# Kernel optimization log

Hardware: AMD Instinct MI355X
Metric: run time of the kernel (lower is better)

## Reference

```python
import jax, jax.numpy as jnp
import numpy as np
import math

EMBED_DIM = 2048
NUM_HEADS = 32
NUM_KV_HEADS = 8
HEAD_DIM = EMBED_DIM // NUM_HEADS  # 64
N_REP = NUM_HEADS // NUM_KV_HEADS  # 4
BATCH = 2
SEQ = 2048


def _rope_tables(seq_len, head_dim):
    # standard RoPE tables matching rotate_half convention (frequencies tiled twice)
    inv_freq = 1.0 / (10000.0 ** (np.arange(0, head_dim, 2, dtype=np.float32) / head_dim))
    t = np.arange(seq_len, dtype=np.float32)
    freqs = np.outer(t, inv_freq)                      # (seq, head_dim/2)
    emb = np.concatenate([freqs, freqs], axis=-1)      # (seq, head_dim)
    return jnp.asarray(np.cos(emb)), jnp.asarray(np.sin(emb))


def setup_inputs() -> dict:
    key = jax.random.key(0)
    ks = jax.random.split(key, 6)
    scale = 1.0 / math.sqrt(EMBED_DIM)
    x = jax.random.normal(ks[0], (BATCH, SEQ, EMBED_DIM), dtype=jnp.float32)
    wq = jax.random.normal(ks[1], (EMBED_DIM, EMBED_DIM), dtype=jnp.float32) * scale
    wk = jax.random.normal(ks[2], (NUM_KV_HEADS * HEAD_DIM, EMBED_DIM), dtype=jnp.float32) * scale
    wv = jax.random.normal(ks[3], (NUM_KV_HEADS * HEAD_DIM, EMBED_DIM), dtype=jnp.float32) * scale
    wo = jax.random.normal(ks[4], (EMBED_DIM, EMBED_DIM), dtype=jnp.float32) * scale
    freqs_cos, freqs_sin = _rope_tables(SEQ, HEAD_DIM)
    return {"x": x, "freqs_cos": freqs_cos, "freqs_sin": freqs_sin,
            "wq": wq, "wk": wk, "wv": wv, "wo": wo}


def _rotate_half(t):
    h = t.shape[-1] // 2
    return jnp.concatenate([-t[..., h:], t[..., :h]], axis=-1)


def reference(x, freqs_cos, freqs_sin, wq, wk, wv, wo):
    b, s, _ = x.shape
    # QKV projections (Linear with weight (out,in): y = x @ W^T)
    xq = (x @ wq.T).reshape(b, s, NUM_HEADS, HEAD_DIM).transpose(0, 2, 1, 3)     # (b,H,s,d)
    xk = (x @ wk.T).reshape(b, s, NUM_KV_HEADS, HEAD_DIM).transpose(0, 2, 1, 3)  # (b,Hkv,s,d)
    xv = (x @ wv.T).reshape(b, s, NUM_KV_HEADS, HEAD_DIM).transpose(0, 2, 1, 3)
    # RoPE: cos/sin (s,d) broadcast over (b,h,s,d)
    xq = xq * freqs_cos + _rotate_half(xq) * freqs_sin
    xk = xk * freqs_cos + _rotate_half(xk) * freqs_sin
    # GQA: repeat_interleave kv heads to match q heads
    xk = jnp.repeat(xk, N_REP, axis=1)  # (b,H,s,d)
    xv = jnp.repeat(xv, N_REP, axis=1)
    scores = jnp.einsum('bhqd,bhkd->bhqk', xq, xk) / math.sqrt(HEAD_DIM)
    causal = jnp.tril(jnp.ones((s, s), dtype=bool))
    scores = jnp.where(causal, scores, jnp.float32(-1e30))
    attn = jax.nn.softmax(scores, axis=-1)
    out = jnp.einsum('bhqk,bhkd->bhqd', attn, xv)        # (b,H,s,d)
    out = out.transpose(0, 2, 1, 3).reshape(b, s, EMBED_DIM)
    return out @ wo.T
```

## Files before the change

kernel.cpp:

```cpp
#include <hip/hip_runtime.h>

#define BATCH 2
#define SEQ 2048
#define EMBED 2048
#define NHEADS 32
#define NKV 8
#define HDIM 64
#define QKV_LD 3072
#define LOG2E 1.44269504088896f

typedef __attribute__((ext_vector_type(8))) short short8;
typedef __attribute__((ext_vector_type(4))) float f32x4;

__device__ inline float hw_exp2(float x) { return __builtin_amdgcn_exp2f(x); }

__device__ inline ushort f2bf(float f) {
  union { float f; unsigned u; } v{f};
  unsigned r = v.u + 0x7FFF + ((v.u >> 16) & 1);
  return (ushort)(r >> 16);
}
__device__ inline float bf2f(ushort u) {
  union { unsigned u; float f; } v{((unsigned)u) << 16};
  return v.f;
}
__device__ inline unsigned fbits(float f) {
  union { float f; unsigned u; } v{f};
  return v.u;
}

__device__ inline void gload16(const ushort* g, ushort* l) {
  __builtin_amdgcn_global_load_lds(
      (const __attribute__((address_space(1))) unsigned*)g,
      (__attribute__((address_space(3))) unsigned*)l, 16, 0, 0);
}

__global__ __launch_bounds__(256) void cvt_all(const float* __restrict__ x,
                                               const float* __restrict__ wq,
                                               const float* __restrict__ wk,
                                               const float* __restrict__ wv,
                                               const float* __restrict__ wo,
                                               ushort* __restrict__ xb,
                                               ushort* __restrict__ wqkv,
                                               ushort* __restrict__ wob) {
  size_t e = (size_t)(blockIdx.x * blockDim.x + threadIdx.x) * 8;
  const float* src;
  ushort* dst;
  if (e < 8388608u) { src = x + e; dst = xb + e; }
  else if (e < 12582912u) { size_t o = e - 8388608u; src = wq + o; dst = wqkv + o; }
  else if (e < 13631488u) { size_t o = e - 12582912u; src = wk + o; dst = wqkv + 4194304u + o; }
  else if (e < 14680064u) { size_t o = e - 13631488u; src = wv + o; dst = wqkv + 5242880u + o; }
  else { size_t o = e - 14680064u; src = wo + o; dst = wob + o; }
  float4 v0 = ((const float4*)src)[0];
  float4 v1 = ((const float4*)src)[1];
  union { uint4 v; ushort u[8]; } pk;
  pk.u[0] = f2bf(v0.x); pk.u[1] = f2bf(v0.y); pk.u[2] = f2bf(v0.z); pk.u[3] = f2bf(v0.w);
  pk.u[4] = f2bf(v1.x); pk.u[5] = f2bf(v1.y); pk.u[6] = f2bf(v1.z); pk.u[7] = f2bf(v1.w);
  *(uint4*)dst = pk.v;
}

template <typename OutT>
__global__ __launch_bounds__(256) void gemm_bf16(const ushort* __restrict__ A,
                                                 const ushort* __restrict__ B,
                                                 OutT* __restrict__ C,
                                                 int M, int N, int K) {
  __shared__ ushort As[128][32];
  __shared__ ushort Bs[128][32];
  const int tid = threadIdx.x;
  const int lane = tid & 63, wave = tid >> 6;
  const int quad = lane >> 4, l16 = lane & 15;
  const int m0 = blockIdx.y * 128, n0 = blockIdx.x * 128;
  const int wm = (wave >> 1) * 64, wn = (wave & 1) * 64;
  const int srow = lane >> 2, skq = (lane & 3) * 8;

  f32x4 acc[4][4] = {};
  for (int k0 = 0; k0 < K; k0 += 32) {
    const ushort* ga = A + (size_t)(m0 + wave * 32 + srow) * K + k0 + skq;
    const ushort* gb = B + (size_t)(n0 + wave * 32 + srow) * K + k0 + skq;
    __syncthreads();
    gload16(ga, &As[wave * 32][0]);
    gload16(ga + (size_t)16 * K, &As[wave * 32 + 16][0]);
    gload16(gb, &Bs[wave * 32][0]);
    gload16(gb + (size_t)16 * K, &Bs[wave * 32 + 16][0]);
    __syncthreads();
    short8 af[4], bf[4];
#pragma unroll
    for (int i = 0; i < 4; i++) af[i] = *(short8*)&As[wm + i * 16 + l16][quad * 8];
#pragma unroll
    for (int j = 0; j < 4; j++) bf[j] = *(short8*)&Bs[wn + j * 16 + l16][quad * 8];
#pragma unroll
    for (int i = 0; i < 4; i++)
#pragma unroll
      for (int j = 0; j < 4; j++)
        acc[i][j] = __builtin_amdgcn_mfma_f32_16x16x32_bf16(af[i], bf[j], acc[i][j], 0, 0, 0);
  }
#pragma unroll
  for (int i = 0; i < 4; i++) {
#pragma unroll
    for (int r = 0; r < 4; r++) {
      size_t rg = (size_t)(m0 + wm + i * 16 + quad * 4 + r);
#pragma unroll
      for (int j = 0; j < 4; j++) {
        float v = acc[i][j][r];
        int cg = n0 + wn + j * 16 + l16;
        if constexpr (sizeof(OutT) == 2)
          C[rg * N + cg] = f2bf(v);
        else
          C[rg * N + cg] = v;
      }
    }
  }
}

__global__ __launch_bounds__(256) void rope_qk(ushort* __restrict__ t,
                                               const float* __restrict__ fc,
                                               const float* __restrict__ fs,
                                               int total) {
  int idx = blockIdx.x * blockDim.x + threadIdx.x;
  if (idx >= total) return;
  int g = idx & 3;
  int hh = (idx >> 2) % 40;
  int tok = idx / 160;
  int s = tok & (SEQ - 1);
  float scale = (hh < 32) ? 0.125f * LOG2E : 1.0f;
  ushort* p = t + (size_t)tok * QKV_LD + hh * 64 + g * 8;
  union { uint4 v; ushort u[8]; } lo, hi, olo, ohi;
  lo.v = *(const uint4*)p;
  hi.v = *(const uint4*)(p + 32);
  const float* fcb = fc + s * HDIM + g * 8;
  const float* fsb = fs + s * HDIM + g * 8;
  float4 c0a = ((const float4*)fcb)[0], c0b = ((const float4*)fcb)[1];
  float4 s0a = ((const float4*)fsb)[0], s0b = ((const float4*)fsb)[1];
  float4 c1a = ((const float4*)(fcb + 32))[0], c1b = ((const float4*)(fcb + 32))[1];
  float4 s1a = ((const float4*)(fsb + 32))[0], s1b = ((const float4*)(fsb + 32))[1];
  float cc0[8] = {c0a.x, c0a.y, c0a.z, c0a.w, c0b.x, c0b.y, c0b.z, c0b.w};
  float ss0[8] = {s0a.x, s0a.y, s0a.z, s0a.w, s0b.x, s0b.y, s0b.z, s0b.w};
  float cc1[8] = {c1a.x, c1a.y, c1a.z, c1a.w, c1b.x, c1b.y, c1b.z, c1b.w};
  float ss1[8] = {s1a.x, s1a.y, s1a.z, s1a.w, s1b.x, s1b.y, s1b.z, s1b.w};
#pragma unroll
  for (int j = 0; j < 8; j++) {
    float x0 = bf2f(lo.u[j]), x1 = bf2f(hi.u[j]);
    olo.u[j] = f2bf((x0 * cc0[j] - x1 * ss0[j]) * scale);
    ohi.u[j] = f2bf((x1 * cc1[j] + x0 * ss1[j]) * scale);
  }
  *(uint4*)p = olo.v;
  *(uint4*)(p + 32) = ohi.v;
}

__global__ __launch_bounds__(256) void attn_mfma(const ushort* __restrict__ QKV,
                                                 ushort* __restrict__ O) {
  __shared__ ushort Ks[64][72];
  __shared__ ushort Vt[64][72];
  __shared__ ushort Pw[4][16][72];
  const int tid = threadIdx.x;
  const int lane = tid & 63, wave = tid >> 6;
  const int quad = lane >> 4, l16 = lane & 15;
  const int bh = blockIdx.y;
  const int b = bh >> 5, h = bh & 31, kh = h >> 2;
  const int p = blockIdx.x;
  const int qt[2] = {p, 31 - p};
  const int ntiles = 32 - p;

  short8 qf[2][2];
#pragma unroll
  for (int u = 0; u < 2; u++)
#pragma unroll
    for (int c = 0; c < 2; c++)
      qf[u][c] = *(const short8*)(QKV +
          (size_t)(b * SEQ + qt[u] * 64 + wave * 16 + l16) * QKV_LD +
          h * HDIM + c * 32 + quad * 8);

  f32x4 o[2][4] = {};
  float m[2] = {-INFINITY, -INFINITY}, l[2] = {0.f, 0.f};

  const ushort* Kbase = QKV + (size_t)b * SEQ * QKV_LD + 2048 + kh * HDIM;
  const ushort* Vbase = Kbase + 512;
  const int kp = tid & 31, dg = tid >> 5;
  const int relrow = wave * 16 + l16;

  for (int t = 0; t < ntiles; t++) {
    const int k0 = t * 64;
    __syncthreads();
    {
      const float4* kpp = (const float4*)(Kbase + (size_t)(k0 + lane) * QKV_LD + wave * 16);
      float4 kv0 = kpp[0], kv1 = kpp[1];
      const uint4* va4 = (const uint4*)(Vbase + (size_t)(k0 + 2 * kp) * QKV_LD + dg * 8);
      const uint4* vb4 = (const uint4*)(Vbase + (size_t)(k0 + 2 * kp + 1) * QKV_LD + dg * 8);
      uint4 va = va4[0], vb = vb4[0];
      *(float4*)&Ks[lane][wave * 16] = kv0;
      *(float4*)&Ks[lane][wave * 16 + 8] = kv1;
      const unsigned* vaw = (const unsigned*)&va;
      const unsigned* vbw = (const unsigned*)&vb;
#pragma unroll
      for (int j = 0; j < 8; j++) {
        unsigned pk = (j & 1)
            ? __builtin_amdgcn_perm(vbw[j >> 1], vaw[j >> 1], 0x07060302)
            : __builtin_amdgcn_perm(vbw[j >> 1], vaw[j >> 1], 0x05040100);
        *(unsigned*)&Vt[dg * 8 + j][2 * kp] = pk;
      }
    }
    __syncthreads();

#pragma unroll
    for (int u = 0; u < 2; u++) {
      const int diag = qt[u];
      if (t > diag) continue;

      f32x4 s[4];
#pragma unroll
      for (int nt = 0; nt < 4; nt++) {
        short8 kf0 = *(short8*)&Ks[nt * 16 + l16][quad * 8];
        short8 kf1 = *(short8*)&Ks[nt * 16 + l16][32 + quad * 8];
        f32x4 z = {};
        z = __builtin_amdgcn_mfma_f32_16x16x32_bf16(kf0, qf[u][0], z, 0, 0, 0);
        s[nt] = __builtin_amdgcn_mfma_f32_16x16x32_bf16(kf1, qf[u][1], z, 0, 0, 0);
      }

      if (t == diag) {
#pragma unroll
        for (int nt = 0; nt < 4; nt++)
#pragma unroll
          for (int r = 0; r < 4; r++)
            if (nt * 16 + quad * 4 + r > relrow) s[nt][r] = -INFINITY;
      }

      float mx = -INFINITY;
#pragma unroll
      for (int nt = 0; nt < 4; nt++)
#pragma unroll
        for (int r = 0; r < 4; r++) mx = fmaxf(mx, s[nt][r]);
      mx = fmaxf(mx, __shfl_xor(mx, 16));
      mx = fmaxf(mx, __shfl_xor(mx, 32));
      float mnew = fmaxf(m[u], mx);
      float al = hw_exp2(m[u] - mnew);
      m[u] = mnew;

      float pv[16];
      float psum = 0.f;
#pragma unroll
      for (int nt = 0; nt < 4; nt++)
#pragma unroll
        for (int r = 0; r < 4; r++) {
          float pe = hw_exp2(s[nt][r] - mnew);
          pv[nt * 4 + r] = pe;
          psum += pe;
        }
      psum += __shfl_xor(psum, 16);
      psum += __shfl_xor(psum, 32);
      l[u] = l[u] * al + psum;
#pragma unroll
      for (int dt = 0; dt < 4; dt++)
#pragma unroll
        for (int r = 0; r < 4; r++) o[u][dt][r] *= al;

#pragma unroll
      for (int nt = 0; nt < 4; nt++) {
        unsigned lo = __builtin_amdgcn_perm(fbits(pv[nt * 4 + 1]), fbits(pv[nt * 4 + 0]), 0x07060302);
        unsigned hi = __builtin_amdgcn_perm(fbits(pv[nt * 4 + 3]), fbits(pv[nt * 4 + 2]), 0x07060302);
        uint2 pk; pk.x = lo; pk.y = hi;
        *(uint2*)&Pw[wave][l16][nt * 16 + quad * 4] = pk;
      }
      short8 pf0 = *(short8*)&Pw[wave][l16][quad * 8];
      short8 pf1 = *(short8*)&Pw[wave][l16][32 + quad * 8];
#pragma unroll
      for (int dt = 0; dt < 4; dt++) {
        short8 vf0 = *(short8*)&Vt[dt * 16 + l16][quad * 8];
        short8 vf1 = *(short8*)&Vt[dt * 16 + l16][32 + quad * 8];
        o[u][dt] = __builtin_amdgcn_mfma_f32_16x16x32_bf16(vf0, pf0, o[u][dt], 0, 0, 0);
        o[u][dt] = __builtin_amdgcn_mfma_f32_16x16x32_bf16(vf1, pf1, o[u][dt], 0, 0, 0);
      }
    }
  }

#pragma unroll
  for (int u = 0; u < 2; u++) {
    float inv = 1.0f / l[u];
    size_t rowg = (size_t)(b * SEQ + qt[u] * 64 + wave * 16 + l16) * EMBED + h * HDIM;
#pragma unroll
    for (int dt = 0; dt < 4; dt++) {
      ushort q0 = f2bf(o[u][dt][0] * inv), q1 = f2bf(o[u][dt][1] * inv);
      ushort q2 = f2bf(o[u][dt][2] * inv), q3 = f2bf(o[u][dt][3] * inv);
      uint2 pk;
      pk.x = (unsigned)q0 | ((unsigned)q1 << 16);
      pk.y = (unsigned)q2 | ((unsigned)q3 << 16);
      *(uint2*)&O[rowg + dt * 16 + quad * 4] = pk;
    }
  }
}

extern "C" void kernel_launch(void* const* d_in, const int* in_sizes, int n_in,
                              void* d_out, int out_size, void* d_ws, size_t ws_size,
                              hipStream_t stream) {
  const float* x = (const float*)d_in[0];
  const float* fcos = (const float*)d_in[1];
  const float* fsin = (const float*)d_in[2];
  const float* wq = (const float*)d_in[3];
  const float* wk = (const float*)d_in[4];
  const float* wv = (const float*)d_in[5];
  const float* wo = (const float*)d_in[6];
  float* out = (float*)d_out;

  const int M = BATCH * SEQ;
  ushort* ws = (ushort*)d_ws;
  ushort* xb = ws;
  ushort* wqkv = xb + (size_t)M * EMBED;
  ushort* wob = wqkv + (size_t)QKV_LD * EMBED;
  ushort* QKVb = wob + (size_t)EMBED * EMBED;
  ushort* Ab = QKVb + (size_t)M * QKV_LD;

  dim3 blk(256);
  cvt_all<<<9216, blk, 0, stream>>>(x, wq, wk, wv, wo, xb, wqkv, wob);

  gemm_bf16<ushort><<<dim3(QKV_LD / 128, M / 128), blk, 0, stream>>>(xb, wqkv, QKVb, M, QKV_LD, EMBED);

  {
    int tot = M * 40 * 4;
    rope_qk<<<(tot + 255) / 256, blk, 0, stream>>>(QKVb, fcos, fsin, tot);
  }

  attn_mfma<<<dim3(16, BATCH * NHEADS), blk, 0, stream>>>(QKVb, Ab);

  gemm_bf16<float><<<dim3(EMBED / 128, M / 128), blk, 0, stream>>>(Ab, wob, out, M, EMBED, EMBED);
}
```

Measured before the change: 326.9 us.

## Pipeline attention loop: double-buffer V, direct K fragments, lazy rescale, interleave two q-tiles

Restructures the flash-attention inner loop. V is prefetched one tile ahead into registers and double-buffered in shared memory, K fragments are loaded straight from global memory instead of through LDS, and the loop has one barrier instead of two. The two query tiles are interleaved so their MFMAs share K/V fragments, with s_setprio around the MFMA blocks. The softmax skips the running-max rescale unless the max grows by more than 8 (log2 units), which reduces exp and multiply work but allows probabilities up to 2^8 in bf16. It also adds register pressure.

Result: slower. 391.4 us (+19.7%).

```diff
diff --git a/kernel.cpp b/kernel.cpp
--- a/kernel.cpp
+++ b/kernel.cpp
@@ -148,46 +148,49 @@
 
 __global__ __launch_bounds__(256) void attn_mfma(const ushort* __restrict__ QKV,
                                                  ushort* __restrict__ O) {
-  __shared__ ushort Ks[64][72];
-  __shared__ ushort Vt[64][72];
-  __shared__ ushort Pw[4][16][72];
+  __shared__ ushort Vt[2][64][72];
+  __shared__ ushort Pw[4][2][16][72];
   const int tid = threadIdx.x;
   const int lane = tid & 63, wave = tid >> 6;
   const int quad = lane >> 4, l16 = lane & 15;
   const int bh = blockIdx.y;
   const int b = bh >> 5, h = bh & 31, kh = h >> 2;
   const int p = blockIdx.x;
-  const int qt[2] = {p, 31 - p};
+  const int qt0 = p, qt1 = 31 - p;
   const int ntiles = 32 - p;
 
-  short8 qf[2][2];
-#pragma unroll
-  for (int u = 0; u < 2; u++)
-#pragma unroll
-    for (int c = 0; c < 2; c++)
-      qf[u][c] = *(const short8*)(QKV +
-          (size_t)(b * SEQ + qt[u] * 64 + wave * 16 + l16) * QKV_LD +
-          h * HDIM + c * 32 + quad * 8);
-
-  f32x4 o[2][4] = {};
-  float m[2] = {-INFINITY, -INFINITY}, l[2] = {0.f, 0.f};
+  short8 qf0[2], qf1[2];
+#pragma unroll
+  for (int c = 0; c < 2; c++) {
+    qf0[c] = *(const short8*)(QKV +
+        (size_t)(b * SEQ + qt0 * 64 + wave * 16 + l16) * QKV_LD +
+        h * HDIM + c * 32 + quad * 8);
+    qf1[c] = *(const short8*)(QKV +
+        (size_t)(b * SEQ + qt1 * 64 + wave * 16 + l16) * QKV_LD +
+        h * HDIM + c * 32 + quad * 8);
+  }
+
+  f32x4 o0[4] = {}, o1[4] = {};
+  float m0 = -INFINITY, m1 = -INFINITY, l0 = 0.f, l1 = 0.f;
 
   const ushort* Kbase = QKV + (size_t)b * SEQ * QKV_LD + 2048 + kh * HDIM;
   const ushort* Vbase = Kbase + 512;
   const int kp = tid & 31, dg = tid >> 5;
   const int relrow = wave * 16 + l16;
 
+  uint4 va = *(const uint4*)(Vbase + (size_t)(2 * kp) * QKV_LD + dg * 8);
+  uint4 vb = *(const uint4*)(Vbase + (size_t)(2 * kp + 1) * QKV_LD + dg * 8);
+
   for (int t = 0; t < ntiles; t++) {
     const int k0 = t * 64;
-    __syncthreads();
+    const int cur = t & 1;
+    const bool act0 = (t <= qt0);
+
+    const int tb = (t + 1 < ntiles ? t + 1 : t) * 64;
+    uint4 na = *(const uint4*)(Vbase + (size_t)(tb + 2 * kp) * QKV_LD + dg * 8);
+    uint4 nb = *(const uint4*)(Vbase + (size_t)(tb + 2 * kp + 1) * QKV_LD + dg * 8);
+
     {
-      const float4* kpp = (const float4*)(Kbase + (size_t)(k0 + lane) * QKV_LD + wave * 16);
-      float4 kv0 = kpp[0], kv1 = kpp[1];
-      const uint4* va4 = (const uint4*)(Vbase + (size_t)(k0 + 2 * kp) * QKV_LD + dg * 8);
-      const uint4* vb4 = (const uint4*)(Vbase + (size_t)(k0 + 2 * kp + 1) * QKV_LD + dg * 8);
-      uint4 va = va4[0], vb = vb4[0];
-      *(float4*)&Ks[lane][wave * 16] = kv0;
-      *(float4*)&Ks[lane][wave * 16 + 8] = kv1;
       const unsigned* vaw = (const unsigned*)&va;
       const unsigned* vbw = (const unsigned*)&vb;
 #pragma unroll
@@ -195,90 +198,138 @@
         unsigned pk = (j & 1)
             ? __builtin_amdgcn_perm(vbw[j >> 1], vaw[j >> 1], 0x07060302)
             : __builtin_amdgcn_perm(vbw[j >> 1], vaw[j >> 1], 0x05040100);
-        *(unsigned*)&Vt[dg * 8 + j][2 * kp] = pk;
-      }
-    }
-    __syncthreads();
-
-#pragma unroll
-    for (int u = 0; u < 2; u++) {
-      const int diag = qt[u];
-      if (t > diag) continue;
-
-      f32x4 s[4];
+        *(unsigned*)&Vt[cur][dg * 8 + j][2 * kp] = pk;
+      }
+    }
+
+    short8 kf0[4], kf1[4];
+#pragma unroll
+    for (int nt = 0; nt < 4; nt++) {
+      const ushort* kr = Kbase + (size_t)(k0 + nt * 16 + l16) * QKV_LD + quad * 8;
+      kf0[nt] = *(const short8*)kr;
+      kf1[nt] = *(const short8*)(kr + 32);
+    }
+
+    asm volatile("s_waitcnt lgkmcnt(0)" ::: "memory");
+    __builtin_amdgcn_s_barrier();
+    __builtin_amdgcn_sched_barrier(0);
+
+    f32x4 s0[4], s1[4];
+    __builtin_amdgcn_s_setprio(1);
+#pragma unroll
+    for (int nt = 0; nt < 4; nt++) {
+      f32x4 z = {};
+      z = __builtin_amdgcn_mfma_f32_16x16x32_bf16(kf0[nt], qf1[0], z, 0, 0, 0);
+      s1[nt] = __builtin_amdgcn_mfma_f32_16x16x32_bf16(kf1[nt], qf1[1], z, 0, 0, 0);
+    }
+    if (act0) {
 #pragma unroll
       for (int nt = 0; nt < 4; nt++) {
-        short8 kf0 = *(short8*)&Ks[nt * 16 + l16][quad * 8];
-        short8 kf1 = *(short8*)&Ks[nt * 16 + l16][32 + quad * 8];
         f32x4 z = {};
-        z = __builtin_amdgcn_mfma_f32_16x16x32_bf16(kf0, qf[u][0], z, 0, 0, 0);
-        s[nt] = __builtin_amdgcn_mfma_f32_16x16x32_bf16(kf1, qf[u][1], z, 0, 0, 0);
-      }
-
-      if (t == diag) {
-#pragma unroll
-        for (int nt = 0; nt < 4; nt++)
-#pragma unroll
-          for (int r = 0; r < 4; r++)
-            if (nt * 16 + quad * 4 + r > relrow) s[nt][r] = -INFINITY;
-      }
-
-      float mx = -INFINITY;
+        z = __builtin_amdgcn_mfma_f32_16x16x32_bf16(kf0[nt], qf0[0], z, 0, 0, 0);
+        s0[nt] = __builtin_amdgcn_mfma_f32_16x16x32_bf16(kf1[nt], qf0[1], z, 0, 0, 0);
+      }
+    }
+    __builtin_amdgcn_s_setprio(0);
+
+    if (t == qt1) {
+#pragma unroll
+      for (int nt = 0; nt < 4; nt++)
+#pragma unroll
+        for (int r = 0; r < 4; r++)
+          if (nt * 16 + quad * 4 + r > relrow) s1[nt][r] = -INFINITY;
+    }
+    if (act0 && t == qt0) {
+#pragma unroll
+      for (int nt = 0; nt < 4; nt++)
+#pragma unroll
+        for (int r = 0; r < 4; r++)
+          if (nt * 16 + quad * 4 + r > relrow) s0[nt][r] = -INFINITY;
+    }
+
+    auto smx = [&](f32x4 (&s)[4], float& mm, float& ll, f32x4 (&oo)[4], ushort* pwb) {
+      float mx = s[0][0];
 #pragma unroll
       for (int nt = 0; nt < 4; nt++)
 #pragma unroll
         for (int r = 0; r < 4; r++) mx = fmaxf(mx, s[nt][r]);
       mx = fmaxf(mx, __shfl_xor(mx, 16));
       mx = fmaxf(mx, __shfl_xor(mx, 32));
-      float mnew = fmaxf(m[u], mx);
-      float al = hw_exp2(m[u] - mnew);
-      m[u] = mnew;
-
-      float pv[16];
+      if (!__all(mx <= mm + 8.f)) {
+        float mnew = fmaxf(mm, mx);
+        float al = hw_exp2(mm - mnew);
+        mm = mnew;
+        ll *= al;
+#pragma unroll
+        for (int dt = 0; dt < 4; dt++)
+#pragma unroll
+          for (int r = 0; r < 4; r++) oo[dt][r] *= al;
+      }
       float psum = 0.f;
 #pragma unroll
-      for (int nt = 0; nt < 4; nt++)
-#pragma unroll
-        for (int r = 0; r < 4; r++) {
-          float pe = hw_exp2(s[nt][r] - mnew);
-          pv[nt * 4 + r] = pe;
-          psum += pe;
-        }
+      for (int nt = 0; nt < 4; nt++) {
+        float p0 = hw_exp2(s[nt][0] - mm), p1 = hw_exp2(s[nt][1] - mm);
+        float p2 = hw_exp2(s[nt][2] - mm), p3 = hw_exp2(s[nt][3] - mm);
+        psum += (p0 + p1) + (p2 + p3);
+        unsigned lo = __builtin_amdgcn_perm(fbits(p1), fbits(p0), 0x07060302);
+        unsigned hi = __builtin_amdgcn_perm(fbits(p3), fbits(p2), 0x07060302);
+        uint2 pk; pk.x = lo; pk.y = hi;
+        *(uint2*)(pwb + l16 * 72 + nt * 16 + quad * 4) = pk;
+      }
       psum += __shfl_xor(psum, 16);
       psum += __shfl_xor(psum, 32);
-      l[u] = l[u] * al + psum;
-#pragma unroll
-      for (int dt = 0; dt < 4; dt++)
-#pragma unroll
-        for (int r = 0; r < 4; r++) o[u][dt][r] *= al;
-
-#pragma unroll
-      for (int nt = 0; nt < 4; nt++) {
-        unsigned lo = __builtin_amdgcn_perm(fbits(pv[nt * 4 + 1]), fbits(pv[nt * 4 + 0]), 0x07060302);
-        unsigned hi = __builtin_amdgcn_perm(fbits(pv[nt * 4 + 3]), fbits(pv[nt * 4 + 2]), 0x07060302);
-        uint2 pk; pk.x = lo; pk.y = hi;
-        *(uint2*)&Pw[wave][l16][nt * 16 + quad * 4] = pk;
-      }
-      short8 pf0 = *(short8*)&Pw[wave][l16][quad * 8];
-      short8 pf1 = *(short8*)&Pw[wave][l16][32 + quad * 8];
-#pragma unroll
-      for (int dt = 0; dt < 4; dt++) {
-        short8 vf0 = *(short8*)&Vt[dt * 16 + l16][quad * 8];
-        short8 vf1 = *(short8*)&Vt[dt * 16 + l16][32 + quad * 8];
-        o[u][dt] = __builtin_amdgcn_mfma_f32_16x16x32_bf16(vf0, pf0, o[u][dt], 0, 0, 0);
-        o[u][dt] = __builtin_amdgcn_mfma_f32_16x16x32_bf16(vf1, pf1, o[u][dt], 0, 0, 0);
-      }
-    }
-  }
-
-#pragma unroll
-  for (int u = 0; u < 2; u++) {
-    float inv = 1.0f / l[u];
-    size_t rowg = (size_t)(b * SEQ + qt[u] * 64 + wave * 16 + l16) * EMBED + h * HDIM;
+      ll += psum;
+    };
+    smx(s1, m1, l1, o1, &Pw[wave][1][0][0]);
+    if (act0) smx(s0, m0, l0, o0, &Pw[wave][0][0][0]);
+
+    const ushort* pb1 = &Pw[wave][1][0][0] + l16 * 72;
+    short8 pf1a = *(const short8*)(pb1 + quad * 8);
+    short8 pf1b = *(const short8*)(pb1 + 32 + quad * 8);
+    short8 pf0a = pf1a, pf0b = pf1b;
+    if (act0) {
+      const ushort* pb0 = &Pw[wave][0][0][0] + l16 * 72;
+      pf0a = *(const short8*)(pb0 + quad * 8);
+      pf0b = *(const short8*)(pb0 + 32 + quad * 8);
+    }
+
+    __builtin_amdgcn_s_setprio(1);
 #pragma unroll
     for (int dt = 0; dt < 4; dt++) {
-      ushort q0 = f2bf(o[u][dt][0] * inv), q1 = f2bf(o[u][dt][1] * inv);
-      ushort q2 = f2bf(o[u][dt][2] * inv), q3 = f2bf(o[u][dt][3] * inv);
+      short8 vf0 = *(const short8*)&Vt[cur][dt * 16 + l16][quad * 8];
+      short8 vf1 = *(const short8*)&Vt[cur][dt * 16 + l16][32 + quad * 8];
+      o1[dt] = __builtin_amdgcn_mfma_f32_16x16x32_bf16(vf0, pf1a, o1[dt], 0, 0, 0);
+      o1[dt] = __builtin_amdgcn_mfma_f32_16x16x32_bf16(vf1, pf1b, o1[dt], 0, 0, 0);
+      if (act0) {
+        o0[dt] = __builtin_amdgcn_mfma_f32_16x16x32_bf16(vf0, pf0a, o0[dt], 0, 0, 0);
+        o0[dt] = __builtin_amdgcn_mfma_f32_16x16x32_bf16(vf1, pf0b, o0[dt], 0, 0, 0);
+      }
+    }
+    __builtin_amdgcn_s_setprio(0);
+
+    va = na; vb = nb;
+  }
+
+  {
+    float inv = 1.0f / l1;
+    size_t rowg = (size_t)(b * SEQ + qt1 * 64 + wave * 16 + l16) * EMBED + h * HDIM;
+#pragma unroll
+    for (int dt = 0; dt < 4; dt++) {
+      ushort q0 = f2bf(o1[dt][0] * inv), q1 = f2bf(o1[dt][1] * inv);
+      ushort q2 = f2bf(o1[dt][2] * inv), q3 = f2bf(o1[dt][3] * inv);
+      uint2 pk;
+      pk.x = (unsigned)q0 | ((unsigned)q1 << 16);
+      pk.y = (unsigned)q2 | ((unsigned)q3 << 16);
+      *(uint2*)&O[rowg + dt * 16 + quad * 4] = pk;
+    }
+  }
+  {
+    float inv = 1.0f / l0;
+    size_t rowg = (size_t)(b * SEQ + qt0 * 64 + wave * 16 + l16) * EMBED + h * HDIM;
+#pragma unroll
+    for (int dt = 0; dt < 4; dt++) {
+      ushort q0 = f2bf(o0[dt][0] * inv), q1 = f2bf(o0[dt][1] * inv);
+      ushort q2 = f2bf(o0[dt][2] * inv), q3 = f2bf(o0[dt][3] * inv);
       uint2 pk;
       pk.x = (unsigned)q0 | ((unsigned)q1 << 16);
       pk.y = (unsigned)q2 | ((unsigned)q3 << 16);
```

## Double-buffer K/V tiles with register prefetch and lazy softmax rescaling

Applied to the files above, without the earlier changes.

The K/V tiles move into double-buffered shared memory, and the next tile's global loads are issued into registers before computing on the current one. This lets a single barrier per iteration replace two and hides global load latency. The softmax rescale of the accumulator is skipped unless the running max grows by more than a threshold, which cuts ALU work. MFMA sections are wrapped in s_setprio to favour matrix issue. In exchange, shared memory use and register pressure go up.

Result: slower. 346.0 us (+5.8%).

```diff
diff --git a/kernel.cpp b/kernel.cpp
--- a/kernel.cpp
+++ b/kernel.cpp
@@ -148,8 +148,8 @@
 
 __global__ __launch_bounds__(256) void attn_mfma(const ushort* __restrict__ QKV,
                                                  ushort* __restrict__ O) {
-  __shared__ ushort Ks[64][72];
-  __shared__ ushort Vt[64][72];
+  __shared__ ushort Ks[2][64][72];
+  __shared__ ushort Vt[2][64][72];
   __shared__ ushort Pw[4][16][72];
   const int tid = threadIdx.x;
   const int lane = tid & 63, wave = tid >> 6;
@@ -177,17 +177,22 @@
   const int kp = tid & 31, dg = tid >> 5;
   const int relrow = wave * 16 + l16;
 
+  float4 ka, kb;
+  uint4 va, vb;
+  {
+    const float4* kpp = (const float4*)(Kbase + (size_t)lane * QKV_LD + wave * 16);
+    ka = kpp[0];
+    kb = kpp[1];
+    va = *(const uint4*)(Vbase + (size_t)(2 * kp) * QKV_LD + dg * 8);
+    vb = *(const uint4*)(Vbase + (size_t)(2 * kp + 1) * QKV_LD + dg * 8);
+  }
+
   for (int t = 0; t < ntiles; t++) {
-    const int k0 = t * 64;
-    __syncthreads();
+    const int cur = t & 1;
+
+    *(float4*)&Ks[cur][lane][wave * 16] = ka;
+    *(float4*)&Ks[cur][lane][wave * 16 + 8] = kb;
     {
-      const float4* kpp = (const float4*)(Kbase + (size_t)(k0 + lane) * QKV_LD + wave * 16);
-      float4 kv0 = kpp[0], kv1 = kpp[1];
-      const uint4* va4 = (const uint4*)(Vbase + (size_t)(k0 + 2 * kp) * QKV_LD + dg * 8);
-      const uint4* vb4 = (const uint4*)(Vbase + (size_t)(k0 + 2 * kp + 1) * QKV_LD + dg * 8);
-      uint4 va = va4[0], vb = vb4[0];
-      *(float4*)&Ks[lane][wave * 16] = kv0;
-      *(float4*)&Ks[lane][wave * 16 + 8] = kv1;
       const unsigned* vaw = (const unsigned*)&va;
       const unsigned* vbw = (const unsigned*)&vb;
 #pragma unroll
@@ -195,10 +200,22 @@
         unsigned pk = (j & 1)
             ? __builtin_amdgcn_perm(vbw[j >> 1], vaw[j >> 1], 0x07060302)
             : __builtin_amdgcn_perm(vbw[j >> 1], vaw[j >> 1], 0x05040100);
-        *(unsigned*)&Vt[dg * 8 + j][2 * kp] = pk;
-      }
-    }
-    __syncthreads();
+        *(unsigned*)&Vt[cur][dg * 8 + j][2 * kp] = pk;
+      }
+    }
+
+    {
+      const int tb = (t + 1 < ntiles ? t + 1 : t) * 64;
+      const float4* kpp = (const float4*)(Kbase + (size_t)(tb + lane) * QKV_LD + wave * 16);
+      ka = kpp[0];
+      kb = kpp[1];
+      va = *(const uint4*)(Vbase + (size_t)(tb + 2 * kp) * QKV_LD + dg * 8);
+      vb = *(const uint4*)(Vbase + (size_t)(tb + 2 * kp + 1) * QKV_LD + dg * 8);
+    }
+
+    asm volatile("s_waitcnt lgkmcnt(0)" ::: "memory");
+    __builtin_amdgcn_s_barrier();
+    __builtin_amdgcn_sched_barrier(0);
 
 #pragma unroll
     for (int u = 0; u < 2; u++) {
@@ -206,14 +223,16 @@
       if (t > diag) continue;
 
       f32x4 s[4];
+      __builtin_amdgcn_s_setprio(1);
 #pragma unroll
       for (int nt = 0; nt < 4; nt++) {
-        short8 kf0 = *(short8*)&Ks[nt * 16 + l16][quad * 8];
-        short8 kf1 = *(short8*)&Ks[nt * 16 + l16][32 + quad * 8];
+        short8 kf0 = *(short8*)&Ks[cur][nt * 16 + l16][quad * 8];
+        short8 kf1 = *(short8*)&Ks[cur][nt * 16 + l16][32 + quad * 8];
         f32x4 z = {};
         z = __builtin_amdgcn_mfma_f32_16x16x32_bf16(kf0, qf[u][0], z, 0, 0, 0);
         s[nt] = __builtin_amdgcn_mfma_f32_16x16x32_bf16(kf1, qf[u][1], z, 0, 0, 0);
       }
+      __builtin_amdgcn_s_setprio(0);
 
       if (t == diag) {
 #pragma unroll
@@ -223,51 +242,51 @@
             if (nt * 16 + quad * 4 + r > relrow) s[nt][r] = -INFINITY;
       }
 
-      float mx = -INFINITY;
+      float mx = s[0][0];
 #pragma unroll
       for (int nt = 0; nt < 4; nt++)
 #pragma unroll
         for (int r = 0; r < 4; r++) mx = fmaxf(mx, s[nt][r]);
       mx = fmaxf(mx, __shfl_xor(mx, 16));
       mx = fmaxf(mx, __shfl_xor(mx, 32));
-      float mnew = fmaxf(m[u], mx);
-      float al = hw_exp2(m[u] - mnew);
-      m[u] = mnew;
-
-      float pv[16];
+
+      if (!__all(mx <= m[u] + 8.f)) {
+        float mnew = fmaxf(m[u], mx);
+        float al = hw_exp2(m[u] - mnew);
+        m[u] = mnew;
+        l[u] *= al;
+#pragma unroll
+        for (int dt = 0; dt < 4; dt++)
+#pragma unroll
+          for (int r = 0; r < 4; r++) o[u][dt][r] *= al;
+      }
+
       float psum = 0.f;
 #pragma unroll
-      for (int nt = 0; nt < 4; nt++)
-#pragma unroll
-        for (int r = 0; r < 4; r++) {
-          float pe = hw_exp2(s[nt][r] - mnew);
-          pv[nt * 4 + r] = pe;
-          psum += pe;
-        }
+      for (int nt = 0; nt < 4; nt++) {
+        float p0 = hw_exp2(s[nt][0] - m[u]), p1 = hw_exp2(s[nt][1] - m[u]);
+        float p2 = hw_exp2(s[nt][2] - m[u]), p3 = hw_exp2(s[nt][3] - m[u]);
+        psum += (p0 + p1) + (p2 + p3);
+        unsigned lo = __builtin_amdgcn_perm(fbits(p1), fbits(p0), 0x07060302);
+        unsigned hi = __builtin_amdgcn_perm(fbits(p3), fbits(p2), 0x07060302);
+        uint2 pk; pk.x = lo; pk.y = hi;
+        *(uint2*)&Pw[wave][l16][nt * 16 + quad * 4] = pk;
+      }
       psum += __shfl_xor(psum, 16);
       psum += __shfl_xor(psum, 32);
-      l[u] = l[u] * al + psum;
-#pragma unroll
-      for (int dt = 0; dt < 4; dt++)
-#pragma unroll
-        for (int r = 0; r < 4; r++) o[u][dt][r] *= al;
-
-#pragma unroll
-      for (int nt = 0; nt < 4; nt++) {
-        unsigned lo = __builtin_amdgcn_perm(fbits(pv[nt * 4 + 1]), fbits(pv[nt * 4 + 0]), 0x07060302);
-        unsigned hi = __builtin_amdgcn_perm(fbits(pv[nt * 4 + 3]), fbits(pv[nt * 4 + 2]), 0x07060302);
-        uint2 pk; pk.x = lo; pk.y = hi;
-        *(uint2*)&Pw[wave][l16][nt * 16 + quad * 4] = pk;
-      }
+      l[u] += psum;
+
       short8 pf0 = *(short8*)&Pw[wave][l16][quad * 8];
       short8 pf1 = *(short8*)&Pw[wave][l16][32 + quad * 8];
+      __builtin_amdgcn_s_setprio(1);
 #pragma unroll
       for (int dt = 0; dt < 4; dt++) {
-        short8 vf0 = *(short8*)&Vt[dt * 16 + l16][quad * 8];
-        short8 vf1 = *(short8*)&Vt[dt * 16 + l16][32 + quad * 8];
+        short8 vf0 = *(short8*)&Vt[cur][dt * 16 + l16][quad * 8];
+        short8 vf1 = *(short8*)&Vt[cur][dt * 16 + l16][32 + quad * 8];
         o[u][dt] = __builtin_amdgcn_mfma_f32_16x16x32_bf16(vf0, pf0, o[u][dt], 0, 0, 0);
         o[u][dt] = __builtin_amdgcn_mfma_f32_16x16x32_bf16(vf1, pf1, o[u][dt], 0, 0, 0);
       }
+      __builtin_amdgcn_s_setprio(0);
     }
   }
 
```

## Use one query tile per block, lazy softmax rescale, MFMA priority hints

Applied to the files above, without the earlier changes.

The attention kernel drops the paired query tiles (p and 31-p) per block and launches 32 blocks per head, each handling one tile with heaviest tiles scheduled first. It adds a lazy rescale that skips the O/l rescaling when the new row max is within 8 (log2 units) of the running max, and wraps MFMA sections in s_setprio. Work balance now relies on the hardware scheduler instead of pairing, and each K/V tile load is shared by only one query tile instead of two, which doubles K/V LDS staging traffic.

After: 394.2 us. 1.21x slower.

```diff
diff --git a/kernel.cpp b/kernel.cpp
--- a/kernel.cpp
+++ b/kernel.cpp
@@ -156,21 +156,18 @@
   const int quad = lane >> 4, l16 = lane & 15;
   const int bh = blockIdx.y;
   const int b = bh >> 5, h = bh & 31, kh = h >> 2;
-  const int p = blockIdx.x;
-  const int qt[2] = {p, 31 - p};
-  const int ntiles = 32 - p;
-
-  short8 qf[2][2];
-#pragma unroll
-  for (int u = 0; u < 2; u++)
-#pragma unroll
-    for (int c = 0; c < 2; c++)
-      qf[u][c] = *(const short8*)(QKV +
-          (size_t)(b * SEQ + qt[u] * 64 + wave * 16 + l16) * QKV_LD +
-          h * HDIM + c * 32 + quad * 8);
-
-  f32x4 o[2][4] = {};
-  float m[2] = {-INFINITY, -INFINITY}, l[2] = {0.f, 0.f};
+  const int qt = 31 - blockIdx.x;
+  const int ntiles = qt + 1;
+
+  short8 qf[2];
+#pragma unroll
+  for (int c = 0; c < 2; c++)
+    qf[c] = *(const short8*)(QKV +
+        (size_t)(b * SEQ + qt * 64 + wave * 16 + l16) * QKV_LD +
+        h * HDIM + c * 32 + quad * 8);
+
+  f32x4 o[4] = {};
+  float m = -INFINITY, l = 0.f;
 
   const ushort* Kbase = QKV + (size_t)b * SEQ * QKV_LD + 2048 + kh * HDIM;
   const ushort* Vbase = Kbase + 512;
@@ -200,85 +197,80 @@
     }
     __syncthreads();
 
-#pragma unroll
-    for (int u = 0; u < 2; u++) {
-      const int diag = qt[u];
-      if (t > diag) continue;
-
-      f32x4 s[4];
-#pragma unroll
-      for (int nt = 0; nt < 4; nt++) {
-        short8 kf0 = *(short8*)&Ks[nt * 16 + l16][quad * 8];
-        short8 kf1 = *(short8*)&Ks[nt * 16 + l16][32 + quad * 8];
-        f32x4 z = {};
-        z = __builtin_amdgcn_mfma_f32_16x16x32_bf16(kf0, qf[u][0], z, 0, 0, 0);
-        s[nt] = __builtin_amdgcn_mfma_f32_16x16x32_bf16(kf1, qf[u][1], z, 0, 0, 0);
-      }
-
-      if (t == diag) {
-#pragma unroll
-        for (int nt = 0; nt < 4; nt++)
-#pragma unroll
-          for (int r = 0; r < 4; r++)
-            if (nt * 16 + quad * 4 + r > relrow) s[nt][r] = -INFINITY;
-      }
-
-      float mx = -INFINITY;
+    f32x4 s[4];
+    __builtin_amdgcn_s_setprio(1);
+#pragma unroll
+    for (int nt = 0; nt < 4; nt++) {
+      short8 kf0 = *(short8*)&Ks[nt * 16 + l16][quad * 8];
+      short8 kf1 = *(short8*)&Ks[nt * 16 + l16][32 + quad * 8];
+      f32x4 z = {};
+      z = __builtin_amdgcn_mfma_f32_16x16x32_bf16(kf0, qf[0], z, 0, 0, 0);
+      s[nt] = __builtin_amdgcn_mfma_f32_16x16x32_bf16(kf1, qf[1], z, 0, 0, 0);
+    }
+    __builtin_amdgcn_s_setprio(0);
+
+    if (t == qt) {
 #pragma unroll
       for (int nt = 0; nt < 4; nt++)
 #pragma unroll
-        for (int r = 0; r < 4; r++) mx = fmaxf(mx, s[nt][r]);
-      mx = fmaxf(mx, __shfl_xor(mx, 16));
-      mx = fmaxf(mx, __shfl_xor(mx, 32));
-      float mnew = fmaxf(m[u], mx);
-      float al = hw_exp2(m[u] - mnew);
-      m[u] = mnew;
-
-      float pv[16];
-      float psum = 0.f;
-#pragma unroll
-      for (int nt = 0; nt < 4; nt++)
-#pragma unroll
-        for (int r = 0; r < 4; r++) {
-          float pe = hw_exp2(s[nt][r] - mnew);
-          pv[nt * 4 + r] = pe;
-          psum += pe;
-        }
-      psum += __shfl_xor(psum, 16);
-      psum += __shfl_xor(psum, 32);
-      l[u] = l[u] * al + psum;
+        for (int r = 0; r < 4; r++)
+          if (nt * 16 + quad * 4 + r > relrow) s[nt][r] = -INFINITY;
+    }
+
+    float mx = s[0][0];
+#pragma unroll
+    for (int nt = 0; nt < 4; nt++)
+#pragma unroll
+      for (int r = 0; r < 4; r++) mx = fmaxf(mx, s[nt][r]);
+    mx = fmaxf(mx, __shfl_xor(mx, 16));
+    mx = fmaxf(mx, __shfl_xor(mx, 32));
+
+    if (!__all(mx <= m + 8.f)) {
+      float mnew = fmaxf(m, mx);
+      float al = hw_exp2(m - mnew);
+      m = mnew;
+      l *= al;
 #pragma unroll
       for (int dt = 0; dt < 4; dt++)
 #pragma unroll
-        for (int r = 0; r < 4; r++) o[u][dt][r] *= al;
-
-#pragma unroll
-      for (int nt = 0; nt < 4; nt++) {
-        unsigned lo = __builtin_amdgcn_perm(fbits(pv[nt * 4 + 1]), fbits(pv[nt * 4 + 0]), 0x07060302);
-        unsigned hi = __builtin_amdgcn_perm(fbits(pv[nt * 4 + 3]), fbits(pv[nt * 4 + 2]), 0x07060302);
-        uint2 pk; pk.x = lo; pk.y = hi;
-        *(uint2*)&Pw[wave][l16][nt * 16 + quad * 4] = pk;
-      }
-      short8 pf0 = *(short8*)&Pw[wave][l16][quad * 8];
-      short8 pf1 = *(short8*)&Pw[wave][l16][32 + quad * 8];
-#pragma unroll
-      for (int dt = 0; dt < 4; dt++) {
-        short8 vf0 = *(short8*)&Vt[dt * 16 + l16][quad * 8];
-        short8 vf1 = *(short8*)&Vt[dt * 16 + l16][32 + quad * 8];
-        o[u][dt] = __builtin_amdgcn_mfma_f32_16x16x32_bf16(vf0, pf0, o[u][dt], 0, 0, 0);
-        o[u][dt] = __builtin_amdgcn_mfma_f32_16x16x32_bf16(vf1, pf1, o[u][dt], 0, 0, 0);
-      }
-    }
-  }
-
-#pragma unroll
-  for (int u = 0; u < 2; u++) {
-    float inv = 1.0f / l[u];
-    size_t rowg = (size_t)(b * SEQ + qt[u] * 64 + wave * 16 + l16) * EMBED + h * HDIM;
+        for (int r = 0; r < 4; r++) o[dt][r] *= al;
+    }
+
+    float psum = 0.f;
+#pragma unroll
+    for (int nt = 0; nt < 4; nt++) {
+      float p0 = hw_exp2(s[nt][0] - m), p1 = hw_exp2(s[nt][1] - m);
+      float p2 = hw_exp2(s[nt][2] - m), p3 = hw_exp2(s[nt][3] - m);
+      psum += (p0 + p1) + (p2 + p3);
+      unsigned lo = __builtin_amdgcn_perm(fbits(p1), fbits(p0), 0x07060302);
+      unsigned hi = __builtin_amdgcn_perm(fbits(p3), fbits(p2), 0x07060302);
+      uint2 pk; pk.x = lo; pk.y = hi;
+      *(uint2*)&Pw[wave][l16][nt * 16 + quad * 4] = pk;
+    }
+    psum += __shfl_xor(psum, 16);
+    psum += __shfl_xor(psum, 32);
+    l += psum;
+
+    short8 pf0 = *(short8*)&Pw[wave][l16][quad * 8];
+    short8 pf1 = *(short8*)&Pw[wave][l16][32 + quad * 8];
+    __builtin_amdgcn_s_setprio(1);
 #pragma unroll
     for (int dt = 0; dt < 4; dt++) {
-      ushort q0 = f2bf(o[u][dt][0] * inv), q1 = f2bf(o[u][dt][1] * inv);
-      ushort q2 = f2bf(o[u][dt][2] * inv), q3 = f2bf(o[u][dt][3] * inv);
+      short8 vf0 = *(short8*)&Vt[dt * 16 + l16][quad * 8];
+      short8 vf1 = *(short8*)&Vt[dt * 16 + l16][32 + quad * 8];
+      o[dt] = __builtin_amdgcn_mfma_f32_16x16x32_bf16(vf0, pf0, o[dt], 0, 0, 0);
+      o[dt] = __builtin_amdgcn_mfma_f32_16x16x32_bf16(vf1, pf1, o[dt], 0, 0, 0);
+    }
+    __builtin_amdgcn_s_setprio(0);
+  }
+
+  {
+    float inv = 1.0f / l;
+    size_t rowg = (size_t)(b * SEQ + qt * 64 + wave * 16 + l16) * EMBED + h * HDIM;
+#pragma unroll
+    for (int dt = 0; dt < 4; dt++) {
+      ushort q0 = f2bf(o[dt][0] * inv), q1 = f2bf(o[dt][1] * inv);
+      ushort q2 = f2bf(o[dt][2] * inv), q3 = f2bf(o[dt][3] * inv);
       uint2 pk;
       pk.x = (unsigned)q0 | ((unsigned)q1 << 16);
       pk.y = (unsigned)q2 | ((unsigned)q3 << 16);
@@ -317,7 +309,7 @@
     rope_qk<<<(tot + 255) / 256, blk, 0, stream>>>(QKVb, fcos, fsin, tot);
   }
 
-  attn_mfma<<<dim3(16, BATCH * NHEADS), blk, 0, stream>>>(QKVb, Ab);
+  attn_mfma<<<dim3(32, BATCH * NHEADS), blk, 0, stream>>>(QKVb, Ab);
 
   gemm_bf16<float><<<dim3(EMBED / 128, M / 128), blk, 0, stream>>>(Ab, wob, out, M, EMBED, EMBED);
 }
```
